# Performance work log

Hardware: AMD Instinct MI355X
Metric: run time of the kernel (lower is better)

Reference implementation:

```python
import jax, jax.numpy as jnp
import numpy as np

B, S, D, H = 8, 2048, 1024, 128  # batch, seq (== CONTEXT_WINDOW), embed dim, headspace


def setup_inputs() -> dict:
    key = jax.random.key(0)
    ks = jax.random.split(key, 7)
    scale = 1.0 / np.sqrt(D)
    return {
        "x": jax.random.normal(ks[0], (B, S, D), dtype=jnp.float32),
        "Wq": jax.random.normal(ks[1], (D, H), dtype=jnp.float32) * scale,
        "bq": jax.random.normal(ks[2], (H,), dtype=jnp.float32) * 0.01,
        "Wk": jax.random.normal(ks[3], (D, H), dtype=jnp.float32) * scale,
        "bk": jax.random.normal(ks[4], (H,), dtype=jnp.float32) * 0.01,
        "Wv": jax.random.normal(ks[5], (D, H), dtype=jnp.float32) * scale,
        "bv": jax.random.normal(ks[6], (H,), dtype=jnp.float32) * 0.01,
    }


def reference(x, Wq, bq, Wk, bk, Wv, bv):
    # x: [B, S, D]
    embedlen = x.shape[-1]
    q = x @ Wq + bq  # [B, S, H]
    k = x @ Wk + bk  # [B, S, H]
    v = x @ Wv + bv  # [B, S, H]
    # NOTE: original code MULTIPLIES by sqrt(embedlen) (embedlen = full embed dim) --
    # faithful reproduction of the source, not the standard 1/sqrt(head_dim).
    scale = jnp.sqrt(jnp.asarray(embedlen, dtype=x.dtype))
    scores = jnp.einsum("bsh,bth->bst", q, k) * scale  # [B, S, S]
    seqlen = x.shape[1]
    causal = jnp.tril(jnp.ones((seqlen, seqlen), dtype=bool))
    scores = jnp.where(causal, scores, -jnp.inf)
    attn = jax.nn.softmax(scores, axis=-1)
    return jnp.einsum("bst,bth->bsh", attn, v)  # [B, S, H]
```

## Files before the change

### kernel.cpp

```cpp
#include <hip/hip_runtime.h>
#include <math.h>

#define SEQ 2048
#define DIM 1024
#define HD  128
#define NB  8
#define M_TOT (NB * SEQ)

typedef __attribute__((ext_vector_type(8))) short   short8;
typedef __attribute__((ext_vector_type(4))) float   floatx4;

__device__ __forceinline__ unsigned short f2bf(float f) {
    unsigned u = __builtin_bit_cast(unsigned, f);
    u += 0x7FFFu + ((u >> 16) & 1u);
    return (unsigned short)(u >> 16);
}
__device__ __forceinline__ float bf2f(unsigned short h) {
    unsigned u = ((unsigned)h) << 16;
    return __builtin_bit_cast(float, u);
}
__device__ __forceinline__ void async16(const void* g, void* l) {
    __builtin_amdgcn_global_load_lds(
        (const __attribute__((address_space(1))) unsigned int*)g,
        (__attribute__((address_space(3))) unsigned int*)l, 16, 0, 0);
}

#define MFMA16(a, b, c) __builtin_amdgcn_mfma_f32_16x16x32_bf16((a), (b), (c), 0, 0, 0)

__global__ __launch_bounds__(256) void wt_prep(
    const float* __restrict__ Wq, const float* __restrict__ Wk, const float* __restrict__ Wv,
    unsigned short* __restrict__ Wth, unsigned short* __restrict__ Wtl)
{
    int idx = blockIdx.x * 256 + threadIdx.x;
    int k   = idx & 1023;
    int n   = (idx >> 10) & 127;
    int mat = idx >> 17;
    const float* W = (mat == 0) ? Wq : (mat == 1) ? Wk : Wv;
    float v = W[k * HD + n];
    unsigned short hi = f2bf(v);
    Wth[idx] = hi;
    Wtl[idx] = f2bf(v - bf2f(hi));
}

__global__ __launch_bounds__(256) void qkv_gemm(
    const float* __restrict__ x,
    const unsigned short* __restrict__ Wth, const unsigned short* __restrict__ Wtl,
    const float* __restrict__ bq, const float* __restrict__ bk, const float* __restrict__ bv,
    unsigned short* __restrict__ Qh, unsigned short* __restrict__ Ql,
    unsigned short* __restrict__ Kh, unsigned short* __restrict__ Kl,
    unsigned short* __restrict__ Vt)
{
    __shared__ short lds[48 * 512];

    const int t    = threadIdx.x;
    const int lane = t & 63;
    const int w    = t >> 6;
    const int lrow = lane & 15;
    const int quad = lane >> 4;

    const int mat = blockIdx.x;
    const int R0  = blockIdx.y * 64;
    const int mh  = w & 1;
    const int nh  = w >> 1;

    floatx4 acc[2][4];
    const floatx4 zf = {0.f, 0.f, 0.f, 0.f};
    #pragma unroll
    for (int i = 0; i < 2; ++i)
        #pragma unroll
        for (int j = 0; j < 4; ++j) acc[i][j] = zf;

    const size_t wmat = (size_t)mat * (HD * DIM);

    auto stage = [&](int k0, int q) {
        const float* xp = x + (size_t)(R0 + w * 16 + lrow) * DIM + k0 + quad * 8;
        float4 xa = *(const float4*)xp;
        float4 xb = *(const float4*)(xp + 4);
        float xv[8] = {xa.x, xa.y, xa.z, xa.w, xb.x, xb.y, xb.z, xb.w};
        short8 hv, lv;
        #pragma unroll
        for (int i = 0; i < 8; ++i) {
            unsigned short h = f2bf(xv[i]);
            hv[i] = (short)h;
            lv[i] = (short)f2bf(xv[i] - bf2f(h));
        }
        *(short8*)&lds[(q * 24 + w * 2 + 0) * 512 + lane * 8] = hv;
        *(short8*)&lds[(q * 24 + w * 2 + 1) * 512 + lane * 8] = lv;
        #pragma unroll
        for (int i = 0; i < 4; ++i) {
            int id = w * 4 + i;
            int p = id & 1, nf = id >> 1;
            const unsigned short* src = (p ? Wtl : Wth) + wmat
                + (size_t)(nf * 16 + lrow) * DIM + k0 + quad * 8;
            async16(src, &lds[(q * 24 + 8 + id) * 512 + lane * 8]);
        }
    };

    stage(0, 0);
    for (int it = 0; it < 32; ++it) {
        __syncthreads();
        if (it < 31) stage((it + 1) * 32, (it + 1) & 1);
        const int q = it & 1;

        short8 a[2][2];
        #pragma unroll
        for (int mi = 0; mi < 2; ++mi)
            #pragma unroll
            for (int p = 0; p < 2; ++p)
                a[mi][p] = *(short8*)&lds[(q * 24 + (2 * mh + mi) * 2 + p) * 512 + lane * 8];

        #pragma unroll
        for (int ni = 0; ni < 4; ++ni) {
            int nf = nh * 4 + ni;
            short8 bh = *(short8*)&lds[(q * 24 + 8 + nf * 2 + 0) * 512 + lane * 8];
            #pragma unroll
            for (int mi = 0; mi < 2; ++mi)
                acc[mi][ni] = MFMA16(a[mi][0], bh, acc[mi][ni]);
            if (mat < 2) {
                short8 bl = *(short8*)&lds[(q * 24 + 8 + nf * 2 + 1) * 512 + lane * 8];
                #pragma unroll
                for (int mi = 0; mi < 2; ++mi) {
                    acc[mi][ni] = MFMA16(a[mi][0], bl, acc[mi][ni]);
                    acc[mi][ni] = MFMA16(a[mi][1], bh, acc[mi][ni]);
                }
            }
        }
    }

    const float* bias = (mat == 0) ? bq : (mat == 1) ? bk : bv;
    #pragma unroll
    for (int ni = 0; ni < 4; ++ni) {
        int col = (nh * 4 + ni) * 16 + lrow;
        float bval = bias[col];
        #pragma unroll
        for (int mi = 0; mi < 2; ++mi) {
            #pragma unroll
            for (int reg = 0; reg < 4; ++reg) {
                int gm = R0 + (2 * mh + mi) * 16 + quad * 4 + reg;
                float v = acc[mi][ni][reg] + bval;
                if (mat == 0) {
                    v *= 32.0f;
                    unsigned short h = f2bf(v);
                    Qh[(size_t)gm * HD + col] = h;
                    Ql[(size_t)gm * HD + col] = f2bf(v - bf2f(h));
                } else if (mat == 1) {
                    unsigned short h = f2bf(v);
                    Kh[(size_t)gm * HD + col] = h;
                    Kl[(size_t)gm * HD + col] = f2bf(v - bf2f(h));
                } else {
                    int b = gm >> 11, s = gm & 2047;
                    Vt[((size_t)b * HD + col) * SEQ + s] = f2bf(v);
                }
            }
        }
    }
}

__global__ __launch_bounds__(256) void flash_attn(
    const unsigned short* __restrict__ Qh, const unsigned short* __restrict__ Ql,
    const unsigned short* __restrict__ Kh, const unsigned short* __restrict__ Kl,
    const unsigned short* __restrict__ Vt, float* __restrict__ out,
    float* __restrict__ Opart, float* __restrict__ ML, int split)
{
    __shared__ short lds[52 * 512];

    const int t    = threadIdx.x;
    const int lane = t & 63;
    const int w    = t >> 6;
    const int lrow = lane & 15;
    const int quad = lane >> 4;

    const int idx = blockIdx.x;
    const int b   = idx & 7;
    const int h   = split ? ((idx >> 3) & 1) : 0;
    const int s   = split ? (63 - (idx >> 4)) : (63 - (idx >> 3));
    const int T   = (s + 2) >> 1;
    const int Th  = (T + 1) >> 1;
    const int t0  = split ? (h ? Th : 0) : 0;
    const int t1  = split ? (h ? T : Th) : T;

    if (split && t0 >= t1) {
        float* op = Opart + (size_t)idx * 4096;
        for (int i = t; i < 4096; i += 256) op[i] = 0.0f;
        if (t < 32) { ML[(idx * 32 + t) * 2] = -1e30f; ML[(idx * 32 + t) * 2 + 1] = 0.0f; }
        return;
    }

    const int mh = w & 1;
    const int kh = w >> 1;
    const int R  = s * 32 + mh * 16;

    const size_t kbase = (size_t)b * SEQ * HD;
    const size_t vbase = (size_t)b * HD * SEQ;

    short8 qf[4][2];
    #pragma unroll
    for (int kc = 0; kc < 4; ++kc) {
        size_t off = kbase + (size_t)(R + lrow) * HD + kc * 32 + quad * 8;
        qf[kc][0] = *(const short8*)(Qh + off);
        qf[kc][1] = *(const short8*)(Ql + off);
    }

    const floatx4 zf = {0.f, 0.f, 0.f, 0.f};
    floatx4 accO[8];
    #pragma unroll
    for (int i = 0; i < 8; ++i) accO[i] = zf;
    float m_[4] = {-1e30f, -1e30f, -1e30f, -1e30f};
    float l_[4] = {0.f, 0.f, 0.f, 0.f};

    for (int it = t0; it < t1; ++it) {
        const int j0 = it * 64;
        __syncthreads();
        #pragma unroll
        for (int i = 0; i < 12; ++i) {
            int id = w * 12 + i;
            const unsigned short* src;
            if (id < 32) {
                int nt = id >> 3, kc = (id >> 1) & 3, p = id & 1;
                src = (p ? Kl : Kh) + kbase
                    + (size_t)(j0 + nt * 16 + lrow) * HD + kc * 32 + quad * 8;
            } else {
                int v = id - 32, df = v >> 1, kc = v & 1;
                src = Vt + vbase + (size_t)(df * 16 + lrow) * SEQ
                    + j0 + kc * 32 + quad * 8;
            }
            async16(src, &lds[id * 512 + lane * 8]);
        }
        __syncthreads();

        floatx4 S[2] = {zf, zf};
        #pragma unroll
        for (int ntl = 0; ntl < 2; ++ntl) {
            int nt = kh * 2 + ntl;
            #pragma unroll
            for (int kc = 0; kc < 4; ++kc) {
                short8 khf = *(short8*)&lds[(nt * 8 + kc * 2 + 0) * 512 + lane * 8];
                short8 klf = *(short8*)&lds[(nt * 8 + kc * 2 + 1) * 512 + lane * 8];
                S[ntl] = MFMA16(qf[kc][0], khf, S[ntl]);
                S[ntl] = MFMA16(qf[kc][0], klf, S[ntl]);
                S[ntl] = MFMA16(qf[kc][1], khf, S[ntl]);
            }
        }
        if (j0 + kh * 32 + 31 > R) {
            #pragma unroll
            for (int ntl = 0; ntl < 2; ++ntl) {
                int key = j0 + (kh * 2 + ntl) * 16 + lrow;
                #pragma unroll
                for (int reg = 0; reg < 4; ++reg) {
                    if (key > R + quad * 4 + reg) S[ntl][reg] = -INFINITY;
                }
            }
        }
        float alpha[4];
        #pragma unroll
        for (int reg = 0; reg < 4; ++reg) {
            float mx = fmaxf(S[0][reg], S[1][reg]);
            #pragma unroll
            for (int hh = 1; hh < 16; hh <<= 1) mx = fmaxf(mx, __shfl_xor(mx, hh));
            float mnew = fmaxf(fmaxf(m_[reg], mx), -1e30f);
            alpha[reg] = __expf(m_[reg] - mnew);
            m_[reg] = mnew;
            float p0 = __expf(S[0][reg] - mnew);
            float p1 = __expf(S[1][reg] - mnew);
            S[0][reg] = p0; S[1][reg] = p1;
            float ls = p0 + p1;
            #pragma unroll
            for (int hh = 1; hh < 16; hh <<= 1) ls += __shfl_xor(ls, hh);
            l_[reg] = l_[reg] * alpha[reg] + ls;
        }
        #pragma unroll
        for (int i = 0; i < 8; ++i)
            #pragma unroll
            for (int reg = 0; reg < 4; ++reg) accO[i][reg] *= alpha[reg];

        #pragma unroll
        for (int ntl = 0; ntl < 2; ++ntl) {
            #pragma unroll
            for (int reg = 0; reg < 4; ++reg) {
                int kloc = ntl * 16 + lrow;
                int jj = kloc & 7, q2 = (kloc >> 3) & 3;
                int lane2 = (quad * 4 + reg) + (q2 << 4);
                lds[(48 + w) * 512 + lane2 * 8 + jj] = (short)f2bf(S[ntl][reg]);
            }
        }
        short8 pf = *(short8*)&lds[(48 + w) * 512 + lane * 8];
        #pragma unroll
        for (int df = 0; df < 8; ++df) {
            short8 vf = *(short8*)&lds[(32 + df * 2 + kh) * 512 + lane * 8];
            accO[df] = MFMA16(pf, vf, accO[df]);
        }
    }

    __syncthreads();
    float* fl   = (float*)lds;
    float* Obuf = fl;
    float* mlb  = fl + 4096;
    if (lrow == 0) {
        #pragma unroll
        for (int reg = 0; reg < 4; ++reg) {
            int row = quad * 4 + reg;
            mlb[((kh * 2 + mh) * 16 + row) * 2 + 0] = m_[reg];
            mlb[((kh * 2 + mh) * 16 + row) * 2 + 1] = l_[reg];
        }
    }
    __syncthreads();
    float myw[4], Mrow[4], Drow[4];
    #pragma unroll
    for (int reg = 0; reg < 4; ++reg) {
        int row = quad * 4 + reg;
        float mo  = mlb[(((1 - kh) * 2 + mh) * 16 + row) * 2 + 0];
        float lo_ = mlb[(((1 - kh) * 2 + mh) * 16 + row) * 2 + 1];
        float M = fmaxf(m_[reg], mo);
        float d = l_[reg] * __expf(m_[reg] - M) + lo_ * __expf(mo - M);
        Mrow[reg] = M; Drow[reg] = d;
        myw[reg] = split ? __expf(m_[reg] - M) : (__expf(m_[reg] - M) / d);
    }
    if (kh == 0) {
        #pragma unroll
        for (int df = 0; df < 8; ++df)
            #pragma unroll
            for (int reg = 0; reg < 4; ++reg)
                Obuf[(mh * 16 + quad * 4 + reg) * 128 + df * 16 + lrow] =
                    accO[df][reg] * myw[reg];
    }
    __syncthreads();
    if (kh == 1) {
        if (split) {
            float* op = Opart + (size_t)idx * 4096;
            #pragma unroll
            for (int df = 0; df < 8; ++df) {
                #pragma unroll
                for (int reg = 0; reg < 4; ++reg) {
                    int row = mh * 16 + quad * 4 + reg;
                    op[row * 128 + df * 16 + lrow] =
                        Obuf[row * 128 + df * 16 + lrow] + accO[df][reg] * myw[reg];
                }
            }
            if (lrow == 0) {
                #pragma unroll
                for (int reg = 0; reg < 4; ++reg) {
                    int row = mh * 16 + quad * 4 + reg;
                    ML[(idx * 32 + row) * 2 + 0] = Mrow[reg];
                    ML[(idx * 32 + row) * 2 + 1] = Drow[reg];
                }
            }
        } else {
            #pragma unroll
            for (int df = 0; df < 8; ++df) {
                #pragma unroll
                for (int reg = 0; reg < 4; ++reg) {
                    float v = Obuf[(mh * 16 + quad * 4 + reg) * 128 + df * 16 + lrow]
                            + accO[df][reg] * myw[reg];
                    size_t o = ((size_t)(b * SEQ + R + quad * 4 + reg)) * HD + df * 16 + lrow;
                    out[o] = v;
                }
            }
        }
    }
}

__global__ __launch_bounds__(256) void splitk_merge(
    const float* __restrict__ Opart, const float* __restrict__ ML,
    float* __restrict__ out)
{
    int tid = blockIdx.x * 256 + threadIdx.x;
    int row = tid >> 5, c4 = tid & 31;
    int b = row >> 11, r = row & 2047, s = r >> 5, rr = r & 31;
    int i0 = ((63 - s) << 4) + b;
    int i1 = i0 + 8;
    float m0 = ML[(i0 * 32 + rr) * 2], l0 = ML[(i0 * 32 + rr) * 2 + 1];
    float m1 = ML[(i1 * 32 + rr) * 2], l1 = ML[(i1 * 32 + rr) * 2 + 1];
    float M  = fmaxf(m0, m1);
    float w0 = __expf(m0 - M), w1 = __expf(m1 - M);
    float inv = 1.0f / (w0 * l0 + w1 * l1);
    float4 a  = *(const float4*)&Opart[((size_t)i0 * 32 + rr) * 128 + c4 * 4];
    float4 bb = *(const float4*)&Opart[((size_t)i1 * 32 + rr) * 128 + c4 * 4];
    float4 o;
    o.x = (w0 * a.x + w1 * bb.x) * inv;
    o.y = (w0 * a.y + w1 * bb.y) * inv;
    o.z = (w0 * a.z + w1 * bb.z) * inv;
    o.w = (w0 * a.w + w1 * bb.w) * inv;
    *(float4*)&out[(size_t)row * 128 + c4 * 4] = o;
}

extern "C" void kernel_launch(void* const* d_in, const int* in_sizes, int n_in,
                              void* d_out, int out_size, void* d_ws, size_t ws_size,
                              hipStream_t stream) {
    const float* x  = (const float*)d_in[0];
    const float* Wq = (const float*)d_in[1];
    const float* bq = (const float*)d_in[2];
    const float* Wk = (const float*)d_in[3];
    const float* bk = (const float*)d_in[4];
    const float* Wv = (const float*)d_in[5];
    const float* bv = (const float*)d_in[6];
    float* out = (float*)d_out;

    unsigned short* Qh  = (unsigned short*)d_ws;
    unsigned short* Ql  = Qh  + (size_t)M_TOT * HD;
    unsigned short* Kh  = Ql  + (size_t)M_TOT * HD;
    unsigned short* Kl  = Kh  + (size_t)M_TOT * HD;
    unsigned short* Vt  = Kl  + (size_t)M_TOT * HD;
    unsigned short* Wth = Vt  + (size_t)M_TOT * HD;
    unsigned short* Wtl = Wth + (size_t)3 * HD * DIM;
    float* Opart = (float*)(Wtl + (size_t)3 * HD * DIM);
    float* ML    = Opart + (size_t)1024 * 32 * 128;

    const size_t need = 22544384ULL + 16777216ULL + 262144ULL;
    const int split = (ws_size >= need) ? 1 : 0;

    wt_prep<<<(3 * HD * DIM) / 256, 256, 0, stream>>>(Wq, Wk, Wv, Wth, Wtl);
    qkv_gemm<<<dim3(3, 256), 256, 0, stream>>>(x, Wth, Wtl, bq, bk, bv, Qh, Ql, Kh, Kl, Vt);
    flash_attn<<<split ? 1024 : 512, 256, 0, stream>>>(Qh, Ql, Kh, Kl, Vt, out, Opart, ML, split);
    if (split) splitk_merge<<<2048, 256, 0, stream>>>(Opart, ML, out);
}
```

Measured before the change: 240.8 us.

## Load QKV GEMM operands directly from global into registers, dropping LDS staging

The QKV projection GEMM no longer stages x and W tiles through shared memory with barriers. Each wave now loads its own x fragments into double-buffered registers and reads W fragments straight from global memory (relying on L2/cache reuse), converting x to hi/lo bf16 per wave. This removes __syncthreads and LDS traffic, but it duplicates x conversion and global loads across the waves that share rows or columns, and it exposes global latency for the W loads.

Result: slower. 284.6 us (+18.2%).

```diff
diff --git a/kernel.cpp b/kernel.cpp
--- a/kernel.cpp
+++ b/kernel.cpp
@@ -50,8 +50,6 @@
     unsigned short* __restrict__ Kh, unsigned short* __restrict__ Kl,
     unsigned short* __restrict__ Vt)
 {
-    __shared__ short lds[48 * 512];
-
     const int t    = threadIdx.x;
     const int lane = t & 63;
     const int w    = t >> 6;
@@ -63,6 +61,22 @@
     const int mh  = w & 1;
     const int nh  = w >> 1;
 
+    const unsigned short* Wh = Wth + (size_t)mat * (HD * DIM);
+    const unsigned short* Wl = Wtl + (size_t)mat * (HD * DIM);
+
+    const float* xr[2];
+    #pragma unroll
+    for (int mi = 0; mi < 2; ++mi)
+        xr[mi] = x + (size_t)(R0 + (2 * mh + mi) * 16 + lrow) * DIM + quad * 8;
+    const unsigned short* wbh[4];
+    const unsigned short* wbl[4];
+    #pragma unroll
+    for (int ni = 0; ni < 4; ++ni) {
+        size_t off = (size_t)((nh * 4 + ni) * 16 + lrow) * DIM + quad * 8;
+        wbh[ni] = Wh + off;
+        wbl[ni] = Wl + off;
+    }
+
     floatx4 acc[2][4];
     const floatx4 zf = {0.f, 0.f, 0.f, 0.f};
     #pragma unroll
@@ -70,61 +84,56 @@
         #pragma unroll
         for (int j = 0; j < 4; ++j) acc[i][j] = zf;
 
-    const size_t wmat = (size_t)mat * (HD * DIM);
-
-    auto stage = [&](int k0, int q) {
-        const float* xp = x + (size_t)(R0 + w * 16 + lrow) * DIM + k0 + quad * 8;
-        float4 xa = *(const float4*)xp;
-        float4 xb = *(const float4*)(xp + 4);
-        float xv[8] = {xa.x, xa.y, xa.z, xa.w, xb.x, xb.y, xb.z, xb.w};
-        short8 hv, lv;
-        #pragma unroll
-        for (int i = 0; i < 8; ++i) {
-            unsigned short h = f2bf(xv[i]);
-            hv[i] = (short)h;
-            lv[i] = (short)f2bf(xv[i] - bf2f(h));
-        }
-        *(short8*)&lds[(q * 24 + w * 2 + 0) * 512 + lane * 8] = hv;
-        *(short8*)&lds[(q * 24 + w * 2 + 1) * 512 + lane * 8] = lv;
-        #pragma unroll
-        for (int i = 0; i < 4; ++i) {
-            int id = w * 4 + i;
-            int p = id & 1, nf = id >> 1;
-            const unsigned short* src = (p ? Wtl : Wth) + wmat
-                + (size_t)(nf * 16 + lrow) * DIM + k0 + quad * 8;
-            async16(src, &lds[(q * 24 + 8 + id) * 512 + lane * 8]);
+    float4 A[2][4];
+
+    auto loadA = [&](int k, int buf) {
+        #pragma unroll
+        for (int mi = 0; mi < 2; ++mi) {
+            A[buf][mi * 2 + 0] = *(const float4*)(xr[mi] + k);
+            A[buf][mi * 2 + 1] = *(const float4*)(xr[mi] + k + 4);
         }
     };
 
-    stage(0, 0);
-    for (int it = 0; it < 32; ++it) {
-        __syncthreads();
-        if (it < 31) stage((it + 1) * 32, (it + 1) & 1);
-        const int q = it & 1;
-
-        short8 a[2][2];
-        #pragma unroll
-        for (int mi = 0; mi < 2; ++mi)
-            #pragma unroll
-            for (int p = 0; p < 2; ++p)
-                a[mi][p] = *(short8*)&lds[(q * 24 + (2 * mh + mi) * 2 + p) * 512 + lane * 8];
-
+    auto compute = [&](int k, int buf) {
+        short8 BH[4], BL[4];
         #pragma unroll
         for (int ni = 0; ni < 4; ++ni) {
-            int nf = nh * 4 + ni;
-            short8 bh = *(short8*)&lds[(q * 24 + 8 + nf * 2 + 0) * 512 + lane * 8];
+            BH[ni] = *(const short8*)(wbh[ni] + k);
+            if (mat < 2) BL[ni] = *(const short8*)(wbl[ni] + k);
+        }
+        short8 ah[2], al[2];
+        #pragma unroll
+        for (int mi = 0; mi < 2; ++mi) {
+            float xv[8] = {A[buf][mi*2].x,   A[buf][mi*2].y,   A[buf][mi*2].z,   A[buf][mi*2].w,
+                           A[buf][mi*2+1].x, A[buf][mi*2+1].y, A[buf][mi*2+1].z, A[buf][mi*2+1].w};
+            #pragma unroll
+            for (int i = 0; i < 8; ++i) {
+                unsigned short h = f2bf(xv[i]);
+                ah[mi][i] = (short)h;
+                al[mi][i] = (short)f2bf(xv[i] - bf2f(h));
+            }
+        }
+        #pragma unroll
+        for (int ni = 0; ni < 4; ++ni) {
             #pragma unroll
             for (int mi = 0; mi < 2; ++mi)
-                acc[mi][ni] = MFMA16(a[mi][0], bh, acc[mi][ni]);
+                acc[mi][ni] = MFMA16(ah[mi], BH[ni], acc[mi][ni]);
             if (mat < 2) {
-                short8 bl = *(short8*)&lds[(q * 24 + 8 + nf * 2 + 1) * 512 + lane * 8];
                 #pragma unroll
                 for (int mi = 0; mi < 2; ++mi) {
-                    acc[mi][ni] = MFMA16(a[mi][0], bl, acc[mi][ni]);
-                    acc[mi][ni] = MFMA16(a[mi][1], bh, acc[mi][ni]);
-                }
-            }
-        }
+                    acc[mi][ni] = MFMA16(ah[mi], BL[ni], acc[mi][ni]);
+                    acc[mi][ni] = MFMA16(al[mi], BH[ni], acc[mi][ni]);
+                }
+            }
+        }
+    };
+
+    loadA(0, 0);
+    for (int it = 0; it < 32; it += 2) {
+        if (it + 1 < 32) loadA((it + 1) * 32, 1);
+        compute(it * 32, 0);
+        if (it + 2 < 32) loadA((it + 2) * 32, 0);
+        compute((it + 1) * 32, 1);
     }
 
     const float* bias = (mat == 0) ? bq : (mat == 1) ? bk : bv;
```

## Double-buffer attention K/V tiles, widen query blocks, async-load x in QKV GEMM

Applied to the files above, without the earlier changes.

The attention kernel now gives each of its 4 waves its own 16 query rows (64 rows per block) and walks 32-key tiles through a double-buffered LDS pipeline. Prefetching the next K/V tile overlaps with compute, and the intra-block key-split merge with its extra LDS reduction and barriers is gone. The QKV GEMM loads x as raw fp32 into LDS with async global-to-LDS copies and does the bf16 hi/lo split after the LDS read, taking the conversion off the staging path. The trade-offs are half as many attention blocks, which lowers parallelism and makes the causal load less even, and redundant conversions of x per wave in the GEMM.

Result: slower. 246.0 us (+2.2%).

```diff
diff --git a/kernel.cpp b/kernel.cpp
--- a/kernel.cpp
+++ b/kernel.cpp
@@ -73,26 +73,19 @@
     const size_t wmat = (size_t)mat * (HD * DIM);
 
     auto stage = [&](int k0, int q) {
-        const float* xp = x + (size_t)(R0 + w * 16 + lrow) * DIM + k0 + quad * 8;
-        float4 xa = *(const float4*)xp;
-        float4 xb = *(const float4*)(xp + 4);
-        float xv[8] = {xa.x, xa.y, xa.z, xa.w, xb.x, xb.y, xb.z, xb.w};
-        short8 hv, lv;
-        #pragma unroll
-        for (int i = 0; i < 8; ++i) {
-            unsigned short h = f2bf(xv[i]);
-            hv[i] = (short)h;
-            lv[i] = (short)f2bf(xv[i] - bf2f(h));
-        }
-        *(short8*)&lds[(q * 24 + w * 2 + 0) * 512 + lane * 8] = hv;
-        *(short8*)&lds[(q * 24 + w * 2 + 1) * 512 + lane * 8] = lv;
-        #pragma unroll
-        for (int i = 0; i < 4; ++i) {
-            int id = w * 4 + i;
-            int p = id & 1, nf = id >> 1;
-            const unsigned short* src = (p ? Wtl : Wth) + wmat
-                + (size_t)(nf * 16 + lrow) * DIM + k0 + quad * 8;
-            async16(src, &lds[(q * 24 + 8 + id) * 512 + lane * 8]);
+        #pragma unroll
+        for (int i = 0; i < 6; ++i) {
+            int id = w * 6 + i;
+            const void* src;
+            if (id < 8) {
+                int mf = id >> 1, c = id & 1;
+                src = x + (size_t)(R0 + mf * 16 + lrow) * DIM + k0 + quad * 8 + c * 4;
+            } else {
+                int bid = id - 8, p = bid & 1, nf = bid >> 1;
+                src = (p ? Wtl : Wth) + wmat
+                    + (size_t)(nf * 16 + lrow) * DIM + k0 + quad * 8;
+            }
+            async16(src, &lds[(q * 24 + id) * 512 + lane * 8]);
         }
     };
 
@@ -102,26 +95,35 @@
         if (it < 31) stage((it + 1) * 32, (it + 1) & 1);
         const int q = it & 1;
 
-        short8 a[2][2];
-        #pragma unroll
-        for (int mi = 0; mi < 2; ++mi)
-            #pragma unroll
-            for (int p = 0; p < 2; ++p)
-                a[mi][p] = *(short8*)&lds[(q * 24 + (2 * mh + mi) * 2 + p) * 512 + lane * 8];
-
+        short8 ah[2], al[2];
+        #pragma unroll
+        for (int mi = 0; mi < 2; ++mi) {
+            int mf = 2 * mh + mi;
+            const float* f0 = (const float*)&lds[(q * 24 + mf * 2 + 0) * 512];
+            const float* f1 = (const float*)&lds[(q * 24 + mf * 2 + 1) * 512];
+            float4 fa = *(const float4*)&f0[lane * 4];
+            float4 fb = *(const float4*)&f1[lane * 4];
+            float xv[8] = {fa.x, fa.y, fa.z, fa.w, fb.x, fb.y, fb.z, fb.w};
+            #pragma unroll
+            for (int i = 0; i < 8; ++i) {
+                unsigned short h = f2bf(xv[i]);
+                ah[mi][i] = (short)h;
+                al[mi][i] = (short)f2bf(xv[i] - bf2f(h));
+            }
+        }
         #pragma unroll
         for (int ni = 0; ni < 4; ++ni) {
             int nf = nh * 4 + ni;
             short8 bh = *(short8*)&lds[(q * 24 + 8 + nf * 2 + 0) * 512 + lane * 8];
             #pragma unroll
             for (int mi = 0; mi < 2; ++mi)
-                acc[mi][ni] = MFMA16(a[mi][0], bh, acc[mi][ni]);
+                acc[mi][ni] = MFMA16(ah[mi], bh, acc[mi][ni]);
             if (mat < 2) {
                 short8 bl = *(short8*)&lds[(q * 24 + 8 + nf * 2 + 1) * 512 + lane * 8];
                 #pragma unroll
                 for (int mi = 0; mi < 2; ++mi) {
-                    acc[mi][ni] = MFMA16(a[mi][0], bl, acc[mi][ni]);
-                    acc[mi][ni] = MFMA16(a[mi][1], bh, acc[mi][ni]);
+                    acc[mi][ni] = MFMA16(ah[mi], bl, acc[mi][ni]);
+                    acc[mi][ni] = MFMA16(al[mi], bh, acc[mi][ni]);
                 }
             }
         }
@@ -173,22 +175,11 @@
     const int idx = blockIdx.x;
     const int b   = idx & 7;
     const int h   = split ? ((idx >> 3) & 1) : 0;
-    const int s   = split ? (63 - (idx >> 4)) : (63 - (idx >> 3));
-    const int T   = (s + 2) >> 1;
-    const int Th  = (T + 1) >> 1;
-    const int t0  = split ? (h ? Th : 0) : 0;
-    const int t1  = split ? (h ? T : Th) : T;
-
-    if (split && t0 >= t1) {
-        float* op = Opart + (size_t)idx * 4096;
-        for (int i = t; i < 4096; i += 256) op[i] = 0.0f;
-        if (t < 32) { ML[(idx * 32 + t) * 2] = -1e30f; ML[(idx * 32 + t) * 2 + 1] = 0.0f; }
-        return;
-    }
-
-    const int mh = w & 1;
-    const int kh = w >> 1;
-    const int R  = s * 32 + mh * 16;
+    const int s   = split ? (31 - (idx >> 4)) : (31 - (idx >> 3));
+    const int t0  = split ? (h * (s + 1)) : 0;
+    const int t1  = t0 + (split ? (s + 1) : (2 * (s + 1)));
+
+    const int R = s * 64 + w * 16;
 
     const size_t kbase = (size_t)b * SEQ * HD;
     const size_t vbase = (size_t)b * HD * SEQ;
@@ -208,152 +199,123 @@
     float m_[4] = {-1e30f, -1e30f, -1e30f, -1e30f};
     float l_[4] = {0.f, 0.f, 0.f, 0.f};
 
-    for (int it = t0; it < t1; ++it) {
-        const int j0 = it * 64;
-        __syncthreads();
-        #pragma unroll
-        for (int i = 0; i < 12; ++i) {
-            int id = w * 12 + i;
+    auto stage = [&](int tile, int q) {
+        const int j0 = tile * 32;
+        #pragma unroll
+        for (int i = 0; i < 6; ++i) {
+            int id = w * 6 + i;
             const unsigned short* src;
-            if (id < 32) {
+            if (id < 16) {
                 int nt = id >> 3, kc = (id >> 1) & 3, p = id & 1;
                 src = (p ? Kl : Kh) + kbase
                     + (size_t)(j0 + nt * 16 + lrow) * HD + kc * 32 + quad * 8;
             } else {
-                int v = id - 32, df = v >> 1, kc = v & 1;
-                src = Vt + vbase + (size_t)(df * 16 + lrow) * SEQ
-                    + j0 + kc * 32 + quad * 8;
-            }
-            async16(src, &lds[id * 512 + lane * 8]);
-        }
+                int df = id - 16;
+                src = Vt + vbase + (size_t)(df * 16 + lrow) * SEQ + j0 + quad * 8;
+            }
+            async16(src, &lds[(q * 24 + id) * 512 + lane * 8]);
+        }
+    };
+
+    stage(t0, 0);
+    for (int it = t0; it < t1; ++it) {
         __syncthreads();
-
-        floatx4 S[2] = {zf, zf};
-        #pragma unroll
-        for (int ntl = 0; ntl < 2; ++ntl) {
-            int nt = kh * 2 + ntl;
-            #pragma unroll
-            for (int kc = 0; kc < 4; ++kc) {
-                short8 khf = *(short8*)&lds[(nt * 8 + kc * 2 + 0) * 512 + lane * 8];
-                short8 klf = *(short8*)&lds[(nt * 8 + kc * 2 + 1) * 512 + lane * 8];
-                S[ntl] = MFMA16(qf[kc][0], khf, S[ntl]);
-                S[ntl] = MFMA16(qf[kc][0], klf, S[ntl]);
-                S[ntl] = MFMA16(qf[kc][1], khf, S[ntl]);
-            }
-        }
-        if (j0 + kh * 32 + 31 > R) {
-            #pragma unroll
-            for (int ntl = 0; ntl < 2; ++ntl) {
-                int key = j0 + (kh * 2 + ntl) * 16 + lrow;
+        if (it + 1 < t1) stage(it + 1, (it + 1 - t0) & 1);
+        const int q  = (it - t0) & 1;
+        const int j0 = it * 32;
+
+        if (j0 <= R + 15) {
+            floatx4 S[2] = {zf, zf};
+            #pragma unroll
+            for (int nt = 0; nt < 2; ++nt) {
+                #pragma unroll
+                for (int kc = 0; kc < 4; ++kc) {
+                    short8 khf = *(short8*)&lds[(q * 24 + nt * 8 + kc * 2 + 0) * 512 + lane * 8];
+                    short8 klf = *(short8*)&lds[(q * 24 + nt * 8 + kc * 2 + 1) * 512 + lane * 8];
+                    S[nt] = MFMA16(qf[kc][0], khf, S[nt]);
+                    S[nt] = MFMA16(qf[kc][0], klf, S[nt]);
+                    S[nt] = MFMA16(qf[kc][1], khf, S[nt]);
+                }
+            }
+            if (j0 + 31 > R) {
+                #pragma unroll
+                for (int nt = 0; nt < 2; ++nt) {
+                    int key = j0 + nt * 16 + lrow;
+                    #pragma unroll
+                    for (int reg = 0; reg < 4; ++reg) {
+                        if (key > R + quad * 4 + reg) S[nt][reg] = -INFINITY;
+                    }
+                }
+            }
+            float alpha[4];
+            #pragma unroll
+            for (int reg = 0; reg < 4; ++reg) {
+                float mx = fmaxf(S[0][reg], S[1][reg]);
+                #pragma unroll
+                for (int hh = 1; hh < 16; hh <<= 1) mx = fmaxf(mx, __shfl_xor(mx, hh));
+                float mnew = fmaxf(fmaxf(m_[reg], mx), -1e30f);
+                alpha[reg] = __expf(m_[reg] - mnew);
+                m_[reg] = mnew;
+                float p0 = __expf(S[0][reg] - mnew);
+                float p1 = __expf(S[1][reg] - mnew);
+                S[0][reg] = p0; S[1][reg] = p1;
+                float ls = p0 + p1;
+                #pragma unroll
+                for (int hh = 1; hh < 16; hh <<= 1) ls += __shfl_xor(ls, hh);
+                l_[reg] = l_[reg] * alpha[reg] + ls;
+            }
+            #pragma unroll
+            for (int i = 0; i < 8; ++i)
+                #pragma unroll
+                for (int reg = 0; reg < 4; ++reg) accO[i][reg] *= alpha[reg];
+
+            #pragma unroll
+            for (int nt = 0; nt < 2; ++nt) {
                 #pragma unroll
                 for (int reg = 0; reg < 4; ++reg) {
-                    if (key > R + quad * 4 + reg) S[ntl][reg] = -INFINITY;
-                }
-            }
-        }
-        float alpha[4];
-        #pragma unroll
-        for (int reg = 0; reg < 4; ++reg) {
-            float mx = fmaxf(S[0][reg], S[1][reg]);
-            #pragma unroll
-            for (int hh = 1; hh < 16; hh <<= 1) mx = fmaxf(mx, __shfl_xor(mx, hh));
-            float mnew = fmaxf(fmaxf(m_[reg], mx), -1e30f);
-            alpha[reg] = __expf(m_[reg] - mnew);
-            m_[reg] = mnew;
-            float p0 = __expf(S[0][reg] - mnew);
-            float p1 = __expf(S[1][reg] - mnew);
-            S[0][reg] = p0; S[1][reg] = p1;
-            float ls = p0 + p1;
-            #pragma unroll
-            for (int hh = 1; hh < 16; hh <<= 1) ls += __shfl_xor(ls, hh);
-            l_[reg] = l_[reg] * alpha[reg] + ls;
-        }
-        #pragma unroll
-        for (int i = 0; i < 8; ++i)
-            #pragma unroll
-            for (int reg = 0; reg < 4; ++reg) accO[i][reg] *= alpha[reg];
-
-        #pragma unroll
-        for (int ntl = 0; ntl < 2; ++ntl) {
-            #pragma unroll
-            for (int reg = 0; reg < 4; ++reg) {
-                int kloc = ntl * 16 + lrow;
-                int jj = kloc & 7, q2 = (kloc >> 3) & 3;
-                int lane2 = (quad * 4 + reg) + (q2 << 4);
-                lds[(48 + w) * 512 + lane2 * 8 + jj] = (short)f2bf(S[ntl][reg]);
-            }
-        }
-        short8 pf = *(short8*)&lds[(48 + w) * 512 + lane * 8];
+                    int kloc = nt * 16 + lrow;
+                    int jj = kloc & 7, q2 = (kloc >> 3) & 3;
+                    int lane2 = (quad * 4 + reg) + (q2 << 4);
+                    lds[(48 + w) * 512 + lane2 * 8 + jj] = (short)f2bf(S[nt][reg]);
+                }
+            }
+            short8 pf = *(short8*)&lds[(48 + w) * 512 + lane * 8];
+            #pragma unroll
+            for (int df = 0; df < 8; ++df) {
+                short8 vf = *(short8*)&lds[(q * 24 + 16 + df) * 512 + lane * 8];
+                accO[df] = MFMA16(pf, vf, accO[df]);
+            }
+        }
+    }
+
+    if (split) {
+        float* op = Opart + (size_t)idx * (64 * 128);
         #pragma unroll
         for (int df = 0; df < 8; ++df) {
-            short8 vf = *(short8*)&lds[(32 + df * 2 + kh) * 512 + lane * 8];
-            accO[df] = MFMA16(pf, vf, accO[df]);
-        }
-    }
-
-    __syncthreads();
-    float* fl   = (float*)lds;
-    float* Obuf = fl;
-    float* mlb  = fl + 4096;
-    if (lrow == 0) {
-        #pragma unroll
-        for (int reg = 0; reg < 4; ++reg) {
-            int row = quad * 4 + reg;
-            mlb[((kh * 2 + mh) * 16 + row) * 2 + 0] = m_[reg];
-            mlb[((kh * 2 + mh) * 16 + row) * 2 + 1] = l_[reg];
-        }
-    }
-    __syncthreads();
-    float myw[4], Mrow[4], Drow[4];
-    #pragma unroll
-    for (int reg = 0; reg < 4; ++reg) {
-        int row = quad * 4 + reg;
-        float mo  = mlb[(((1 - kh) * 2 + mh) * 16 + row) * 2 + 0];
-        float lo_ = mlb[(((1 - kh) * 2 + mh) * 16 + row) * 2 + 1];
-        float M = fmaxf(m_[reg], mo);
-        float d = l_[reg] * __expf(m_[reg] - M) + lo_ * __expf(mo - M);
-        Mrow[reg] = M; Drow[reg] = d;
-        myw[reg] = split ? __expf(m_[reg] - M) : (__expf(m_[reg] - M) / d);
-    }
-    if (kh == 0) {
-        #pragma unroll
-        for (int df = 0; df < 8; ++df)
-            #pragma unroll
-            for (int reg = 0; reg < 4; ++reg)
-                Obuf[(mh * 16 + quad * 4 + reg) * 128 + df * 16 + lrow] =
-                    accO[df][reg] * myw[reg];
-    }
-    __syncthreads();
-    if (kh == 1) {
-        if (split) {
-            float* op = Opart + (size_t)idx * 4096;
-            #pragma unroll
-            for (int df = 0; df < 8; ++df) {
-                #pragma unroll
-                for (int reg = 0; reg < 4; ++reg) {
-                    int row = mh * 16 + quad * 4 + reg;
-                    op[row * 128 + df * 16 + lrow] =
-                        Obuf[row * 128 + df * 16 + lrow] + accO[df][reg] * myw[reg];
-                }
-            }
-            if (lrow == 0) {
-                #pragma unroll
-                for (int reg = 0; reg < 4; ++reg) {
-                    int row = mh * 16 + quad * 4 + reg;
-                    ML[(idx * 32 + row) * 2 + 0] = Mrow[reg];
-                    ML[(idx * 32 + row) * 2 + 1] = Drow[reg];
-                }
-            }
-        } else {
-            #pragma unroll
-            for (int df = 0; df < 8; ++df) {
-                #pragma unroll
-                for (int reg = 0; reg < 4; ++reg) {
-                    float v = Obuf[(mh * 16 + quad * 4 + reg) * 128 + df * 16 + lrow]
-                            + accO[df][reg] * myw[reg];
-                    size_t o = ((size_t)(b * SEQ + R + quad * 4 + reg)) * HD + df * 16 + lrow;
-                    out[o] = v;
-                }
+            #pragma unroll
+            for (int reg = 0; reg < 4; ++reg) {
+                int rl = w * 16 + quad * 4 + reg;
+                op[rl * 128 + df * 16 + lrow] = accO[df][reg];
+            }
+        }
+        if (lrow == 0) {
+            #pragma unroll
+            for (int reg = 0; reg < 4; ++reg) {
+                int rl = w * 16 + quad * 4 + reg;
+                ML[(idx * 64 + rl) * 2 + 0] = m_[reg];
+                ML[(idx * 64 + rl) * 2 + 1] = l_[reg];
+            }
+        }
+    } else {
+        float inv[4];
+        #pragma unroll
+        for (int reg = 0; reg < 4; ++reg) inv[reg] = 1.0f / l_[reg];
+        #pragma unroll
+        for (int df = 0; df < 8; ++df) {
+            #pragma unroll
+            for (int reg = 0; reg < 4; ++reg) {
+                size_t o = ((size_t)(b * SEQ + R + quad * 4 + reg)) * HD + df * 16 + lrow;
+                out[o] = accO[df][reg] * inv[reg];
             }
         }
     }
@@ -365,16 +327,16 @@
 {
     int tid = blockIdx.x * 256 + threadIdx.x;
     int row = tid >> 5, c4 = tid & 31;
-    int b = row >> 11, r = row & 2047, s = r >> 5, rr = r & 31;
-    int i0 = ((63 - s) << 4) + b;
+    int b = row >> 11, r = row & 2047, s = r >> 6, rl = r & 63;
+    int i0 = ((31 - s) << 4) + b;
     int i1 = i0 + 8;
-    float m0 = ML[(i0 * 32 + rr) * 2], l0 = ML[(i0 * 32 + rr) * 2 + 1];
-    float m1 = ML[(i1 * 32 + rr) * 2], l1 = ML[(i1 * 32 + rr) * 2 + 1];
+    float m0 = ML[(i0 * 64 + rl) * 2], l0 = ML[(i0 * 64 + rl) * 2 + 1];
+    float m1 = ML[(i1 * 64 + rl) * 2], l1 = ML[(i1 * 64 + rl) * 2 + 1];
     float M  = fmaxf(m0, m1);
     float w0 = __expf(m0 - M), w1 = __expf(m1 - M);
     float inv = 1.0f / (w0 * l0 + w1 * l1);
-    float4 a  = *(const float4*)&Opart[((size_t)i0 * 32 + rr) * 128 + c4 * 4];
-    float4 bb = *(const float4*)&Opart[((size_t)i1 * 32 + rr) * 128 + c4 * 4];
+    float4 a  = *(const float4*)&Opart[((size_t)i0 * 64 + rl) * 128 + c4 * 4];
+    float4 bb = *(const float4*)&Opart[((size_t)i1 * 64 + rl) * 128 + c4 * 4];
     float4 o;
     o.x = (w0 * a.x + w1 * bb.x) * inv;
     o.y = (w0 * a.y + w1 * bb.y) * inv;
@@ -403,13 +365,13 @@
     unsigned short* Wth = Vt  + (size_t)M_TOT * HD;
     unsigned short* Wtl = Wth + (size_t)3 * HD * DIM;
     float* Opart = (float*)(Wtl + (size_t)3 * HD * DIM);
-    float* ML    = Opart + (size_t)1024 * 32 * 128;
+    float* ML    = Opart + (size_t)512 * 64 * 128;
 
     const size_t need = 22544384ULL + 16777216ULL + 262144ULL;
     const int split = (ws_size >= need) ? 1 : 0;
 
     wt_prep<<<(3 * HD * DIM) / 256, 256, 0, stream>>>(Wq, Wk, Wv, Wth, Wtl);
     qkv_gemm<<<dim3(3, 256), 256, 0, stream>>>(x, Wth, Wtl, bq, bk, bv, Qh, Ql, Kh, Kl, Vt);
-    flash_attn<<<split ? 1024 : 512, 256, 0, stream>>>(Qh, Ql, Kh, Kl, Vt, out, Opart, ML, split);
+    flash_attn<<<split ? 512 : 256, 256, 0, stream>>>(Qh, Ql, Kh, Kl, Vt, out, Opart, ML, split);
     if (split) splitk_merge<<<2048, 256, 0, stream>>>(Opart, ML, out);
 }
```
